# Kernel tuning notes

Measured on AMD Instinct MI355X. Metric: run time of the kernel, lower is better.

Reference implementation:

```python
import jax, jax.numpy as jnp
import numpy as np

N_NODES = 100000
N_EDGES = 1600000
IN_CH = 128
HID_CH = 128
OUT_CH = 64
N_GRAPHS = 256


def setup_inputs() -> dict:
    key = jax.random.key(0)
    ks = jax.random.split(key, 12)
    x = jax.random.normal(ks[0], (N_NODES, IN_CH), dtype=jnp.float32)
    edge_index = jax.random.randint(ks[1], (2, N_EDGES), 0, N_NODES, dtype=jnp.int64)
    batch = jnp.sort(jax.random.randint(ks[2], (N_NODES,), 0, N_GRAPHS, dtype=jnp.int64))
    def lin(k, fin, fout):
        bound = 1.0 / np.sqrt(fin)
        kw, kb = jax.random.split(k)
        W = jax.random.uniform(kw, (fin, fout), minval=-bound, maxval=bound, dtype=jnp.float32)
        b = jax.random.uniform(kb, (fout,), minval=-bound, maxval=bound, dtype=jnp.float32)
        return W, b
    W1, b1 = lin(ks[3], IN_CH, HID_CH)
    W2, b2 = lin(ks[4], HID_CH, HID_CH)
    W3, b3 = lin(ks[5], HID_CH, HID_CH)
    Wf, bf = lin(ks[6], HID_CH, OUT_CH)
    return {"x": x, "edge_index": edge_index, "batch": batch,
            "W1": W1, "b1": b1, "W2": W2, "b2": b2,
            "W3": W3, "b3": b3, "Wf": Wf, "bf": bf}


def _gin_conv(x, src, dst, W, b):
    # GINConv with eps=0: nn((1+eps)*x + sum_{j in N(i)} x_j)
    agg = jax.ops.segment_sum(x[src], dst, num_segments=N_NODES)
    return (x + agg) @ W + b


def reference(x, edge_index, batch, W1, b1, W2, b2, W3, b3, Wf, bf):
    src, dst = edge_index[0], edge_index[1]  # source_to_target flow
    h = jax.nn.relu(_gin_conv(x, src, dst, W1, b1))
    h = jax.nn.relu(_gin_conv(h, src, dst, W2, b2))
    h = jax.nn.relu(_gin_conv(h, src, dst, W3, b3))
    # global_mean_pool over graph ids
    sums = jax.ops.segment_sum(h, batch, num_segments=N_GRAPHS)  # [G, H]
    counts = jax.ops.segment_sum(jnp.ones((h.shape[0],), h.dtype), batch, num_segments=N_GRAPHS)
    pooled = sums / jnp.maximum(counts, 1.0)[:, None]
    # dropout is identity in eval mode
    logits = pooled @ Wf + bf  # [G, OUT_CH]
    return logits
```

## Files before the change

### kernel.cpp

```cpp
#include <hip/hip_runtime.h>

#define N_NODES 100000
#define N_EDGES 1600000
#define N_GRAPHS 256
#define CH 128
#define OUT_CH 64
#define NB 391
#define BCAP 4608
#define CAPN 48

typedef __attribute__((ext_vector_type(8))) short bf16x8;
typedef __attribute__((ext_vector_type(4))) float f32x4;
typedef unsigned short ushort_t;
typedef unsigned int uint_t;
typedef unsigned char u8_t;

static __device__ inline ushort_t f2bf(float f) {
    uint_t u = __float_as_uint(f);
    uint_t r = (u + 0x7FFFu + ((u >> 16) & 1u)) >> 16;
    return (ushort_t)r;
}
static __device__ inline uint_t pack2bf(float x, float y) {
    return (uint_t)f2bf(x) | ((uint_t)f2bf(y) << 16);
}
static __device__ inline float bflo(uint_t v) { return __uint_as_float(v << 16); }
static __device__ inline float bfhi(uint_t v) { return __uint_as_float(v & 0xFFFF0000u); }

static __device__ inline uint_t pack4fp8(float a, float b, float c, float d) {
    int v = __builtin_amdgcn_cvt_pk_fp8_f32(a, b, 0, false);
    v = __builtin_amdgcn_cvt_pk_fp8_f32(c, d, v, true);
    return (uint_t)v;
}
static __device__ inline u8_t f2fp8(float a) {
    return (u8_t)(__builtin_amdgcn_cvt_pk_fp8_f32(a, a, 0, false) & 0xFF);
}


__global__ __launch_bounds__(1024) void k_passA(const int* __restrict__ src, const int* __restrict__ dst,
                                                int* __restrict__ resCnt, uint_t* __restrict__ pairBuf,
                                                const float* __restrict__ x, u8_t* __restrict__ xb,
                                                const float* __restrict__ W1, const float* __restrict__ W2,
                                                const float* __restrict__ W3, ushort_t* __restrict__ WT) {
    int blk = blockIdx.x, tid = threadIdx.x;
    if (blk < 196) {
        __shared__ int hist[NB];
        __shared__ int base[NB];
        for (int t = tid; t < NB; t += 1024) hist[t] = 0;
        __syncthreads();
        uint_t v[8]; int bk[8], rk[8];
        int e0 = blk * 8192;
        #pragma unroll
        for (int j = 0; j < 8; ++j) {
            int e = e0 + j * 1024 + tid;
            bk[j] = -1;
            if (e < N_EDGES) {
                int d = dst[e];
                int s = src[e];
                int b = d >> 8;
                bk[j] = b;
                v[j] = (uint_t)s | ((uint_t)(d & 255) << 17);
                rk[j] = atomicAdd(&hist[b], 1);
            }
        }
        __syncthreads();
        for (int t = tid; t < NB; t += 1024)
            base[t] = atomicAdd(&resCnt[t * 16], hist[t]);
        __syncthreads();
        #pragma unroll
        for (int j = 0; j < 8; ++j) {
            if (bk[j] >= 0) {
                int pos = base[bk[j]] + rk[j];
                if (pos < BCAP) pairBuf[(size_t)bk[j] * BCAP + pos] = v[j];
            }
        }
    } else if (blk < 1759) {
        int i = (blk - 196) * 1024 + tid;
        if (i < N_NODES * 16) {
            const float4* xp = (const float4*)(x) + (size_t)i * 2;
            float4 a = xp[0], bb = xp[1];
            uint2 o;
            o.x = pack4fp8(a.x, a.y, a.z, a.w);
            o.y = pack4fp8(bb.x, bb.y, bb.z, bb.w);
            ((uint2*)xb)[i] = o;
        }
    } else {
        int idx = (blk - 1759) * 1024 + tid;
        int w = idx >> 14;
        int r = idx & 16383;
        const float* W = (w == 0) ? W1 : (w == 1) ? W2 : W3;
        int k = r >> 7, n = r & 127;
        WT[w * 16384 + n * 128 + k] = f2bf(W[r]);
    }
}


__global__ __launch_bounds__(256) void k_passB(const int* __restrict__ resCnt,
                                               const uint_t* __restrict__ pairBuf,
                                               int* __restrict__ cnt, int* __restrict__ col) {
    __shared__ int csr[256 * CAPN];
    __shared__ int lcnt[256];
    int b = blockIdx.x, tid = threadIdx.x;
    lcnt[tid] = 0;
    for (int i = tid; i < 256 * CAPN; i += 256) csr[i] = 0;
    __syncthreads();
    int ce = resCnt[b * 16];
    if (ce > BCAP) ce = BCAP;
    const uint_t* __restrict__ pb = pairBuf + (size_t)b * BCAP;
    for (int i = tid; i < ce; i += 256) {
        uint_t v = pb[i];
        int d = v >> 17;
        int p = atomicAdd(&lcnt[d], 1);
        if (p < CAPN) csr[d * CAPN + p] = (int)(v & 0x1FFFFu);
    }
    __syncthreads();
    int gbase = b * 256;
    int lim = (gbase + 256 <= N_NODES) ? 256 * CAPN : (N_NODES - gbase) * CAPN;
    for (int i = tid; i < lim; i += 256) col[(size_t)gbase * CAPN + i] = csr[i];
    int node = gbase + tid;
    if (node < N_NODES) {
        int c = lcnt[tid];
        cnt[node] = c > CAPN ? CAPN : c;
    }
}


__global__ __launch_bounds__(256) void k_fused(const u8_t* __restrict__ hin,
                                               const int* __restrict__ cnt,
                                               const int* __restrict__ col,
                                               const ushort_t* __restrict__ WT,
                                               const float* __restrict__ bias,
                                               u8_t* __restrict__ Hout,
                                               float* __restrict__ pooled,
                                               const int* __restrict__ batch) {
    __shared__ uint_t ldsZ[16][68];
    __shared__ float ldsO[16][132];

    int tid  = threadIdx.x;
    int w    = tid >> 6;
    int lane = tid & 63;
    int row0 = blockIdx.x * 16;

    int mrow  = lane & 15;
    int kbase = (lane >> 4) * 8;
    int qid   = lane >> 4;
    int sl    = lane & 15;
    int qb    = qid * 16;

    int node = row0 + w * 4 + qid;
    int e = cnt[node];
    int cr0 = col[(size_t)node * CAPN + sl];
    int cr1 = col[(size_t)node * CAPN + 16 + sl];
    int cr2 = col[(size_t)node * CAPN + 32 + sl];

    int emax = e;
    emax = max(emax, __shfl(emax, lane ^ 16));
    emax = max(emax, __shfl(emax, lane ^ 32));

    float f0, f1, f2, f3, f4, f5, f6, f7;
    {
        uint2 sv = *(const uint2*)(hin + (size_t)node * 128 + sl * 8);
        f0 = __builtin_amdgcn_cvt_f32_fp8(sv.x, 0);
        f1 = __builtin_amdgcn_cvt_f32_fp8(sv.x, 1);
        f2 = __builtin_amdgcn_cvt_f32_fp8(sv.x, 2);
        f3 = __builtin_amdgcn_cvt_f32_fp8(sv.x, 3);
        f4 = __builtin_amdgcn_cvt_f32_fp8(sv.y, 0);
        f5 = __builtin_amdgcn_cvt_f32_fp8(sv.y, 1);
        f6 = __builtin_amdgcn_cvt_f32_fp8(sv.y, 2);
        f7 = __builtin_amdgcn_cvt_f32_fp8(sv.y, 3);
    }

#define ACCG(G, V)                                                       \
    f0 = fmaf(G, __builtin_amdgcn_cvt_f32_fp8(V.x, 0), f0);              \
    f1 = fmaf(G, __builtin_amdgcn_cvt_f32_fp8(V.x, 1), f1);              \
    f2 = fmaf(G, __builtin_amdgcn_cvt_f32_fp8(V.x, 2), f2);              \
    f3 = fmaf(G, __builtin_amdgcn_cvt_f32_fp8(V.x, 3), f3);              \
    f4 = fmaf(G, __builtin_amdgcn_cvt_f32_fp8(V.y, 0), f4);              \
    f5 = fmaf(G, __builtin_amdgcn_cvt_f32_fp8(V.y, 1), f5);              \
    f6 = fmaf(G, __builtin_amdgcn_cvt_f32_fp8(V.y, 2), f6);              \
    f7 = fmaf(G, __builtin_amdgcn_cvt_f32_fp8(V.y, 3), f7);

#define CHUNK(CREG, BASE)                                                    \
    if ((BASE) < emax) {                                                     \
        int lim = emax - (BASE); if (lim > 16) lim = 16;                     \
        for (int tt = 0; tt < lim; tt += 4) {                                \
            int i1 = tt + 1, i2 = tt + 2, i3 = tt + 3;                       \
            if (i1 > 15) i1 = 15; if (i2 > 15) i2 = 15; if (i3 > 15) i3 = 15;\
            int c0 = __shfl(CREG, qb + tt);                                  \
            int c1 = __shfl(CREG, qb + i1);                                  \
            int c2 = __shfl(CREG, qb + i2);                                  \
            int c3 = __shfl(CREG, qb + i3);                                  \
            bool v0 = (BASE) + tt     < e;                                   \
            bool v1 = (BASE) + tt + 1 < e;                                   \
            bool v2 = (BASE) + tt + 2 < e;                                   \
            bool v3 = (BASE) + tt + 3 < e;                                   \
            int a0 = v0 ? c0 : node;                                         \
            int a1 = v1 ? c1 : node;                                         \
            int a2 = v2 ? c2 : node;                                         \
            int a3 = v3 ? c3 : node;                                         \
            uint2 x0 = *(const uint2*)(hin + (size_t)a0 * 128 + sl * 8);     \
            uint2 x1 = *(const uint2*)(hin + (size_t)a1 * 128 + sl * 8);     \
            uint2 x2 = *(const uint2*)(hin + (size_t)a2 * 128 + sl * 8);     \
            uint2 x3 = *(const uint2*)(hin + (size_t)a3 * 128 + sl * 8);     \
            float g0 = v0 ? 1.0f : 0.0f;                                     \
            float g1 = v1 ? 1.0f : 0.0f;                                     \
            float g2 = v2 ? 1.0f : 0.0f;                                     \
            float g3 = v3 ? 1.0f : 0.0f;                                     \
            ACCG(g0, x0) ACCG(g1, x1) ACCG(g2, x2) ACCG(g3, x3)              \
        }                                                                    \
    }

    CHUNK(cr0, 0)
    CHUNK(cr1, 16)
    CHUNK(cr2, 32)
#undef CHUNK
#undef ACCG

    {
        uint4 o;
        o.x = pack2bf(f0, f1);
        o.y = pack2bf(f2, f3);
        o.z = pack2bf(f4, f5);
        o.w = pack2bf(f6, f7);
        *(uint4*)&ldsZ[w * 4 + qid][sl * 4] = o;
    }

    __builtin_amdgcn_sched_barrier(0);
    bf16x8 bfr[2][4];
    #pragma unroll
    for (int j = 0; j < 2; ++j) {
        int nt = w * 2 + j;
        #pragma unroll
        for (int kc = 0; kc < 4; ++kc) {
            bfr[j][kc] = *(const bf16x8*)(WT + (size_t)(nt * 16 + mrow) * 128 + kc * 32 + kbase);
        }
    }
    __syncthreads();

    f32x4 acc[2];
    #pragma unroll
    for (int j = 0; j < 2; ++j) { f32x4 zz = {0.f, 0.f, 0.f, 0.f}; acc[j] = zz; }

    const ushort_t* zsh = (const ushort_t*)&ldsZ[0][0];
    #pragma unroll
    for (int kc = 0; kc < 4; ++kc) {
        int k0 = kc * 32 + kbase;
        bf16x8 afrag = *(const bf16x8*)(zsh + mrow * 136 + k0);
        acc[0] = __builtin_amdgcn_mfma_f32_16x16x32_bf16(afrag, bfr[0][kc], acc[0], 0, 0, 0);
        acc[1] = __builtin_amdgcn_mfma_f32_16x16x32_bf16(afrag, bfr[1][kc], acc[1], 0, 0, 0);
    }

    int colbase = lane & 15;
    int rsel = (lane >> 4) * 4;

    if (pooled == nullptr) {
        #pragma unroll
        for (int j = 0; j < 2; ++j) {
            int coln = (w * 2 + j) * 16 + colbase;
            float bv = bias[coln];
            #pragma unroll
            for (int r = 0; r < 4; ++r) {
                float v = fmaxf(acc[j][r] + bv, 0.0f);
                Hout[(size_t)(row0 + rsel + r) * 128 + coln] = f2fp8(v);
            }
        }
    } else {
        #pragma unroll
        for (int j = 0; j < 2; ++j) {
            int coln = (w * 2 + j) * 16 + colbase;
            float bv = bias[coln];
            #pragma unroll
            for (int r = 0; r < 4; ++r) {
                ldsO[rsel + r][coln] = fmaxf(acc[j][r] + bv, 0.0f);
            }
        }
        __syncthreads();
        if (tid < 128) {
            int gprev = batch[row0];
            float run = 0.f;
            #pragma unroll
            for (int r = 0; r < 16; ++r) {
                int gr = batch[row0 + r];
                if (gr != gprev) {
                    atomicAdd(&pooled[gprev * 128 + tid], run);
                    run = 0.f;
                    gprev = gr;
                }
                run += ldsO[r][tid];
            }
            atomicAdd(&pooled[gprev * 128 + tid], run);
        }
    }
}


__global__ __launch_bounds__(64) void k_final(const float* __restrict__ pooled,
                                              const int* __restrict__ batch,
                                              const float* __restrict__ Wf,
                                              const float* __restrict__ bfv,
                                              float* __restrict__ out) {
    __shared__ float pl[128];
    int g = blockIdx.x, t = threadIdx.x;
    int lo = 0, hi = N_NODES;
    while (lo < hi) { int mid = (lo + hi) >> 1; if (batch[mid] < g) lo = mid + 1; else hi = mid; }
    int s = lo;
    lo = 0; hi = N_NODES;
    while (lo < hi) { int mid = (lo + hi) >> 1; if (batch[mid] < g + 1) lo = mid + 1; else hi = mid; }
    float inv = 1.0f / fmaxf((float)(lo - s), 1.0f);
    pl[t] = pooled[g * 128 + t] * inv;
    pl[t + 64] = pooled[g * 128 + t + 64] * inv;
    __syncthreads();
    float acc = bfv[t];
    #pragma unroll 8
    for (int k = 0; k < CH; ++k) acc += pl[k] * Wf[k * 64 + t];
    out[g * 64 + t] = acc;
}

extern "C" void kernel_launch(void* const* d_in, const int* in_sizes, int n_in,
                              void* d_out, int out_size, void* d_ws, size_t ws_size,
                              hipStream_t stream) {
    const float* x   = (const float*)d_in[0];
    const int*   ei  = (const int*)d_in[1];
    const int*   src = ei;
    const int*   dst = ei + N_EDGES;
    const int*   batch = (const int*)d_in[2];
    const float* W1 = (const float*)d_in[3];
    const float* b1 = (const float*)d_in[4];
    const float* W2 = (const float*)d_in[5];
    const float* b2 = (const float*)d_in[6];
    const float* W3 = (const float*)d_in[7];
    const float* b3 = (const float*)d_in[8];
    const float* Wf = (const float*)d_in[9];
    const float* bf = (const float*)d_in[10];
    float* out = (float*)d_out;

    char* p = (char*)d_ws;
    auto alloc = [&](size_t bytes) -> void* {
        void* r = (void*)p;
        p += (bytes + 255) & ~(size_t)255;
        return r;
    };
    int* resCnt = (int*)alloc((size_t)NB * 16 * sizeof(int));
    uint_t* pairBuf = (uint_t*)alloc((size_t)NB * BCAP * sizeof(uint_t));
    int* cnt = (int*)alloc(N_NODES * sizeof(int));
    int* col = (int*)alloc((size_t)(NB * 256) * CAPN * sizeof(int));
    ushort_t* wt = (ushort_t*)alloc(3 * CH * CH * sizeof(ushort_t));
    u8_t* xb = (u8_t*)alloc((size_t)N_NODES * CH);
    u8_t* ha = (u8_t*)alloc((size_t)N_NODES * CH);
    u8_t* hb = (u8_t*)alloc((size_t)N_NODES * CH);
    float* pooled = (float*)alloc((size_t)N_GRAPHS * CH * sizeof(float));

    hipMemsetAsync(resCnt, 0, (size_t)NB * 16 * sizeof(int), stream);
    hipMemsetAsync(pooled, 0, (size_t)N_GRAPHS * CH * sizeof(float), stream);
    k_passA<<<1807, 1024, 0, stream>>>(src, dst, resCnt, pairBuf, x, xb, W1, W2, W3, wt);
    k_passB<<<NB, 256, 0, stream>>>(resCnt, pairBuf, cnt, col);

    const int fusedGrid = N_NODES / 16;

    k_fused<<<fusedGrid, 256, 0, stream>>>(xb, cnt, col, wt,         b1, ha, nullptr, nullptr);
    k_fused<<<fusedGrid, 256, 0, stream>>>(ha, cnt, col, wt + 16384, b2, hb, nullptr, nullptr);
    k_fused<<<fusedGrid, 256, 0, stream>>>(hb, cnt, col, wt + 32768, b3, nullptr, pooled, batch);
    k_final<<<N_GRAPHS, 64, 0, stream>>>(pooled, batch, Wf, bf, out);
}
```

Baseline: 289.1 us.

## Sort nodes by degree to balance gather work across wavefronts

Adds a single-block counting sort that builds a permutation of nodes ordered by in-degree. The first two fused layers process nodes in that order, so the four nodes sharing a wavefront have similar edge counts and the loop bound emax wastes fewer iterations; results are scattered back to their original rows. It also skips loading the unused column chunks, uses packed fp8-to-f32 conversions, and merges the two memsets into one. The sort runs on one block over 100k nodes, which adds a serial step, and the permuted order gives less locality in the row writes.

```diff
diff --git a/kernel.cpp b/kernel.cpp
--- a/kernel.cpp
+++ b/kernel.cpp
@@ -11,6 +11,7 @@
 
 typedef __attribute__((ext_vector_type(8))) short bf16x8;
 typedef __attribute__((ext_vector_type(4))) float f32x4;
+typedef __attribute__((ext_vector_type(2))) float f32x2;
 typedef unsigned short ushort_t;
 typedef unsigned int uint_t;
 typedef unsigned char u8_t;
@@ -23,8 +24,6 @@
 static __device__ inline uint_t pack2bf(float x, float y) {
     return (uint_t)f2bf(x) | ((uint_t)f2bf(y) << 16);
 }
-static __device__ inline float bflo(uint_t v) { return __uint_as_float(v << 16); }
-static __device__ inline float bfhi(uint_t v) { return __uint_as_float(v & 0xFFFF0000u); }
 
 static __device__ inline uint_t pack4fp8(float a, float b, float c, float d) {
     int v = __builtin_amdgcn_cvt_pk_fp8_f32(a, b, 0, false);
@@ -124,6 +123,26 @@
 }
 
 
+__global__ __launch_bounds__(1024) void k_sort(const int* __restrict__ cnt, int* __restrict__ perm) {
+    __shared__ int hist[CAPN + 1];
+    __shared__ int base[CAPN + 1];
+    int tid = threadIdx.x;
+    if (tid <= CAPN) hist[tid] = 0;
+    __syncthreads();
+    for (int i = tid; i < N_NODES; i += 1024) atomicAdd(&hist[cnt[i]], 1);
+    __syncthreads();
+    if (tid == 0) {
+        int s = 0;
+        for (int b = 0; b <= CAPN; ++b) { base[b] = s; s += hist[b]; }
+    }
+    __syncthreads();
+    for (int i = tid; i < N_NODES; i += 1024) {
+        int p = atomicAdd(&base[cnt[i]], 1);
+        perm[p] = i;
+    }
+}
+
+
 __global__ __launch_bounds__(256) void k_fused(const u8_t* __restrict__ hin,
                                                const int* __restrict__ cnt,
                                                const int* __restrict__ col,
@@ -131,9 +150,11 @@
                                                const float* __restrict__ bias,
                                                u8_t* __restrict__ Hout,
                                                float* __restrict__ pooled,
-                                               const int* __restrict__ batch) {
+                                               const int* __restrict__ batch,
+                                               const int* __restrict__ perm) {
     __shared__ uint_t ldsZ[16][68];
     __shared__ float ldsO[16][132];
+    __shared__ int ldsP[16];
 
     int tid  = threadIdx.x;
     int w    = tid >> 6;
@@ -146,11 +167,14 @@
     int sl    = lane & 15;
     int qb    = qid * 16;
 
-    int node = row0 + w * 4 + qid;
+    if (tid < 16) ldsP[tid] = perm ? perm[row0 + tid] : (row0 + tid);
+
+    int prow = row0 + w * 4 + qid;
+    int node = perm ? perm[prow] : prow;
     int e = cnt[node];
     int cr0 = col[(size_t)node * CAPN + sl];
-    int cr1 = col[(size_t)node * CAPN + 16 + sl];
-    int cr2 = col[(size_t)node * CAPN + 32 + sl];
+    int cr1 = (e > 16) ? col[(size_t)node * CAPN + 16 + sl] : 0;
+    int cr2 = (e > 32) ? col[(size_t)node * CAPN + 32 + sl] : 0;
 
     int emax = e;
     emax = max(emax, __shfl(emax, lane ^ 16));
@@ -159,25 +183,25 @@
     float f0, f1, f2, f3, f4, f5, f6, f7;
     {
         uint2 sv = *(const uint2*)(hin + (size_t)node * 128 + sl * 8);
-        f0 = __builtin_amdgcn_cvt_f32_fp8(sv.x, 0);
-        f1 = __builtin_amdgcn_cvt_f32_fp8(sv.x, 1);
-        f2 = __builtin_amdgcn_cvt_f32_fp8(sv.x, 2);
-        f3 = __builtin_amdgcn_cvt_f32_fp8(sv.x, 3);
-        f4 = __builtin_amdgcn_cvt_f32_fp8(sv.y, 0);
-        f5 = __builtin_amdgcn_cvt_f32_fp8(sv.y, 1);
-        f6 = __builtin_amdgcn_cvt_f32_fp8(sv.y, 2);
-        f7 = __builtin_amdgcn_cvt_f32_fp8(sv.y, 3);
+        f32x2 p0 = __builtin_amdgcn_cvt_pk_f32_fp8((int)sv.x, false);
+        f32x2 p1 = __builtin_amdgcn_cvt_pk_f32_fp8((int)sv.x, true);
+        f32x2 p2 = __builtin_amdgcn_cvt_pk_f32_fp8((int)sv.y, false);
+        f32x2 p3 = __builtin_amdgcn_cvt_pk_f32_fp8((int)sv.y, true);
+        f0 = p0.x; f1 = p0.y; f2 = p1.x; f3 = p1.y;
+        f4 = p2.x; f5 = p2.y; f6 = p3.x; f7 = p3.y;
     }
 
 #define ACCG(G, V)                                                       \
-    f0 = fmaf(G, __builtin_amdgcn_cvt_f32_fp8(V.x, 0), f0);              \
-    f1 = fmaf(G, __builtin_amdgcn_cvt_f32_fp8(V.x, 1), f1);              \
-    f2 = fmaf(G, __builtin_amdgcn_cvt_f32_fp8(V.x, 2), f2);              \
-    f3 = fmaf(G, __builtin_amdgcn_cvt_f32_fp8(V.x, 3), f3);              \
-    f4 = fmaf(G, __builtin_amdgcn_cvt_f32_fp8(V.y, 0), f4);              \
-    f5 = fmaf(G, __builtin_amdgcn_cvt_f32_fp8(V.y, 1), f5);              \
-    f6 = fmaf(G, __builtin_amdgcn_cvt_f32_fp8(V.y, 2), f6);              \
-    f7 = fmaf(G, __builtin_amdgcn_cvt_f32_fp8(V.y, 3), f7);
+    {                                                                    \
+        f32x2 p0 = __builtin_amdgcn_cvt_pk_f32_fp8((int)(V).x, false);   \
+        f32x2 p1 = __builtin_amdgcn_cvt_pk_f32_fp8((int)(V).x, true);    \
+        f32x2 p2 = __builtin_amdgcn_cvt_pk_f32_fp8((int)(V).y, false);   \
+        f32x2 p3 = __builtin_amdgcn_cvt_pk_f32_fp8((int)(V).y, true);    \
+        f0 = fmaf(G, p0.x, f0); f1 = fmaf(G, p0.y, f1);                  \
+        f2 = fmaf(G, p1.x, f2); f3 = fmaf(G, p1.y, f3);                  \
+        f4 = fmaf(G, p2.x, f4); f5 = fmaf(G, p2.y, f5);                  \
+        f6 = fmaf(G, p3.x, f6); f7 = fmaf(G, p3.y, f7);                  \
+    }
 
 #define CHUNK(CREG, BASE)                                                    \
     if ((BASE) < emax) {                                                     \
@@ -260,7 +284,8 @@
             #pragma unroll
             for (int r = 0; r < 4; ++r) {
                 float v = fmaxf(acc[j][r] + bv, 0.0f);
-                Hout[(size_t)(row0 + rsel + r) * 128 + coln] = f2fp8(v);
+                int grow = ldsP[rsel + r];
+                Hout[(size_t)grow * 128 + coln] = f2fp8(v);
             }
         }
     } else {
@@ -340,24 +365,26 @@
         return r;
     };
     int* resCnt = (int*)alloc((size_t)NB * 16 * sizeof(int));
+    float* pooled = (float*)alloc((size_t)N_GRAPHS * CH * sizeof(float));
+    size_t zeroBytes = (size_t)((char*)(pooled + N_GRAPHS * CH) - (char*)resCnt);
     uint_t* pairBuf = (uint_t*)alloc((size_t)NB * BCAP * sizeof(uint_t));
     int* cnt = (int*)alloc(N_NODES * sizeof(int));
     int* col = (int*)alloc((size_t)(NB * 256) * CAPN * sizeof(int));
+    int* perm = (int*)alloc(N_NODES * sizeof(int));
     ushort_t* wt = (ushort_t*)alloc(3 * CH * CH * sizeof(ushort_t));
     u8_t* xb = (u8_t*)alloc((size_t)N_NODES * CH);
     u8_t* ha = (u8_t*)alloc((size_t)N_NODES * CH);
     u8_t* hb = (u8_t*)alloc((size_t)N_NODES * CH);
-    float* pooled = (float*)alloc((size_t)N_GRAPHS * CH * sizeof(float));
-
-    hipMemsetAsync(resCnt, 0, (size_t)NB * 16 * sizeof(int), stream);
-    hipMemsetAsync(pooled, 0, (size_t)N_GRAPHS * CH * sizeof(float), stream);
+
+    hipMemsetAsync(resCnt, 0, zeroBytes, stream);
     k_passA<<<1807, 1024, 0, stream>>>(src, dst, resCnt, pairBuf, x, xb, W1, W2, W3, wt);
     k_passB<<<NB, 256, 0, stream>>>(resCnt, pairBuf, cnt, col);
+    k_sort<<<1, 1024, 0, stream>>>(cnt, perm);
 
     const int fusedGrid = N_NODES / 16;
 
-    k_fused<<<fusedGrid, 256, 0, stream>>>(xb, cnt, col, wt,         b1, ha, nullptr, nullptr);
-    k_fused<<<fusedGrid, 256, 0, stream>>>(ha, cnt, col, wt + 16384, b2, hb, nullptr, nullptr);
-    k_fused<<<fusedGrid, 256, 0, stream>>>(hb, cnt, col, wt + 32768, b3, nullptr, pooled, batch);
+    k_fused<<<fusedGrid, 256, 0, stream>>>(xb, cnt, col, wt,         b1, ha, nullptr, nullptr, perm);
+    k_fused<<<fusedGrid, 256, 0, stream>>>(ha, cnt, col, wt + 16384, b2, hb, nullptr, nullptr, perm);
+    k_fused<<<fusedGrid, 256, 0, stream>>>(hb, cnt, col, wt + 32768, b3, nullptr, pooled, batch, nullptr);
     k_final<<<N_GRAPHS, 64, 0, stream>>>(pooled, batch, Wf, bf, out);
 }
```

New measurement: 348.7 us. 1.21x slower.
